# Optimization experiments

Hardware: AMD Instinct MI355X
Metric: run time of the kernel (lower is better)

The kernel has to match this reference:

```python
import jax, jax.numpy as jnp
from jax import lax
import numpy as np

B = 8; L = 1024; D_MODEL = 128; N_LAYER = 4
D_INNER = 256; D_STATE = 16; D_CONV = 4; DT_RANK = 8  # ceil(128/16)
N_STATE = 2; EPS = 1e-5


def setup_inputs() -> dict:
    key = jax.random.key(0)
    ks = jax.random.split(key, 9)
    s = 0.02
    return {
        "x": jax.random.normal(ks[0], (B, L, D_MODEL), jnp.float32),
        "in_proj_w": jax.random.normal(ks[1], (N_LAYER, 2 * D_INNER, D_MODEL), jnp.float32) * s,
        "conv_w": jax.random.normal(ks[2], (N_LAYER, D_INNER, 1, D_CONV), jnp.float32) * s,
        "conv_b": jnp.zeros((N_LAYER, D_INNER), jnp.float32),
        "x_proj_w": jax.random.normal(ks[3], (N_LAYER, DT_RANK + 2 * D_STATE, D_INNER), jnp.float32) * s,
        "dt_proj_w": jax.random.normal(ks[4], (N_LAYER, D_INNER, DT_RANK), jnp.float32) * s,
        "dt_proj_b": jax.random.normal(ks[5], (N_LAYER, D_INNER), jnp.float32) * s,
        "A_log": jnp.log(jnp.tile(jnp.arange(1, D_STATE + 1, dtype=jnp.float32), (N_LAYER, D_INNER, 1))),
        "D_param": jnp.ones((N_LAYER, D_INNER), jnp.float32),
        "out_proj_w": jax.random.normal(ks[6], (N_LAYER, D_MODEL, D_INNER), jnp.float32) * s,
        "norm_w": jnp.ones((N_LAYER, D_MODEL), jnp.float32),
        "norm_f_w": jnp.ones((D_MODEL,), jnp.float32),
        "bn_gamma": jnp.ones((D_MODEL,), jnp.float32),
        "bn_beta": jnp.zeros((D_MODEL,), jnp.float32),
        "head_w": jax.random.normal(ks[7], (N_STATE, D_MODEL), jnp.float32) * s,
        "head_b": jnp.zeros((N_STATE,), jnp.float32),
    }


def _rmsnorm(x, w):
    return x * lax.rsqrt(jnp.mean(x * x, axis=-1, keepdims=True) + EPS) * w


def _selective_scan(u, delta, A, Bm, Cm, D):
    # u, delta: (b,l,d); A: (d,n); Bm, Cm: (b,l,n); D: (d,)
    deltaA = jnp.exp(delta[..., None] * A)                          # (b,l,d,n)
    deltaBu = delta[..., None] * Bm[:, :, None, :] * u[..., None]   # (b,l,d,n)

    def step(h, t):
        dA, dBu, c = t
        h = dA * h + dBu                                            # (b,d,n)
        return h, jnp.einsum('bdn,bn->bd', h, c)

    h0 = jnp.zeros((u.shape[0], u.shape[2], A.shape[1]), u.dtype)
    _, ys = lax.scan(step, h0, (jnp.moveaxis(deltaA, 1, 0),
                                jnp.moveaxis(deltaBu, 1, 0),
                                jnp.moveaxis(Cm, 1, 0)))
    return jnp.moveaxis(ys, 0, 1) + u * D                           # (b,l,d)


def _mamba_block(x, in_w, cw, cb, xp_w, dt_w, dt_b, A_log, Dp, out_w):
    xz = jnp.einsum('bld,ed->ble', x, in_w)                         # (b,l,2*d_inner)
    xs, res = jnp.split(xz, 2, axis=-1)
    # depthwise causal conv, kernel D_CONV, left pad D_CONV-1 (matches pad=3 + truncate)
    xc = lax.conv_general_dilated(jnp.transpose(xs, (0, 2, 1)), cw, (1,),
                                  [(D_CONV - 1, 0)],
                                  dimension_numbers=('NCH', 'OIH', 'NCH'),
                                  feature_group_count=D_INNER)
    xs = jax.nn.silu(jnp.transpose(xc + cb[None, :, None], (0, 2, 1)))
    dbc = jnp.einsum('bld,ed->ble', xs, xp_w)
    dlt, Bm, Cm = jnp.split(dbc, [DT_RANK, DT_RANK + D_STATE], axis=-1)
    delta = jax.nn.softplus(jnp.einsum('blr,dr->bld', dlt, dt_w) + dt_b)
    A = -jnp.exp(A_log)
    y = _selective_scan(xs, delta, A, Bm, Cm, Dp)
    y = y * jax.nn.silu(res)
    return jnp.einsum('ble,de->bld', y, out_w)


def reference(x, in_proj_w, conv_w, conv_b, x_proj_w, dt_proj_w, dt_proj_b,
              A_log, D_param, out_proj_w, norm_w, norm_f_w,
              bn_gamma, bn_beta, head_w, head_b):
    h = x
    for i in range(N_LAYER):
        h = h + _mamba_block(_rmsnorm(h, norm_w[i]), in_proj_w[i], conv_w[i],
                             conv_b[i], x_proj_w[i], dt_proj_w[i], dt_proj_b[i],
                             A_log[i], D_param[i], out_proj_w[i])
    h = _rmsnorm(h, norm_f_w)
    feat = h[:, -1, :]                                              # (b, d_model)
    # BatchNorm1d (training mode: batch stats, biased variance), ReLU, Dropout(eval)=id
    mu = jnp.mean(feat, axis=0)
    var = jnp.mean((feat - mu) ** 2, axis=0)
    feat = (feat - mu) * lax.rsqrt(var + EPS) * bn_gamma + bn_beta
    feat = jax.nn.relu(feat)
    return feat @ head_w.T + head_b                                 # (b, n_state)
```

## Files before the change

kernel.cpp:

```cpp
#include <hip/hip_runtime.h>
#include <cstddef>

#define LQ 1024
#define DM 128
#define DI 256
#define DSN 16
#define NB 8
#define ROWS (NB*LQ)
#define EPSF 1e-5f
#define CHUNK 32
#define NCHUNK (LQ/CHUNK)

typedef _Float16 f16;
typedef __attribute__((ext_vector_type(8))) _Float16 f16x8;
typedef __attribute__((ext_vector_type(4))) _Float16 f16x4;
typedef __attribute__((ext_vector_type(4))) float f32x4;

static __device__ __forceinline__ float sigmoid_f(float x) { return 1.f/(1.f+__expf(-x)); }
static __device__ __forceinline__ float softplus_f(float x) {
  return (x > 20.f) ? x : log1pf(__expf(x));
}

__global__ __launch_bounds__(256) void cvt_all(
    const float* __restrict__ a, const float* __restrict__ bsrc, const float* __restrict__ csrc,
    f16* __restrict__ oa, f16* __restrict__ ob, f16* __restrict__ oc)
{
  int i = blockIdx.x*256 + threadIdx.x;
  const int na = (4*2*DI*DM)/4;
  const int nb = (4*40*DI)/4;
  const int nc = (4*DM*DI)/4;
  const float* s; f16* o; int k;
  if (i < na)            { s = a;    o = oa; k = i; }
  else if (i < na+nb)    { s = bsrc; o = ob; k = i - na; }
  else if (i < na+nb+nc) { s = csrc; o = oc; k = i - na - nb; }
  else return;
  float4 v = ((const float4*)s)[k];
  f16x4 r; r.x=(f16)v.x; r.y=(f16)v.y; r.z=(f16)v.z; r.w=(f16)v.w;
  ((f16x4*)o)[k] = r;
}

__global__ __launch_bounds__(256) void layer_front(
    const float* __restrict__ src, const float* __restrict__ nw,
    const f16* __restrict__ Win,
    const float* __restrict__ cw, const float* __restrict__ cb,
    const f16* __restrict__ xpw,
    const float* __restrict__ A_log,
    const float* __restrict__ dtw, const float* __restrict__ dtb,
    f16* __restrict__ xs_out, float* __restrict__ dbc_out,
    float* __restrict__ S, float* __restrict__ sumdl_out)
{
  __shared__ __align__(16) f16 Ah[48][136];
  __shared__ __align__(16) f16 sXc[48][264];
  __shared__ __align__(16) f16 sXs[32][264];
  __shared__ __align__(16) float sDbc[32][40];
  const int bc = blockIdx.x;
  const int b = bc >> 5, ck = bc & (NCHUNK-1);
  const int t0 = ck*CHUNK;
  const int tid = threadIdx.x;

  {
    const int r = tid >> 2;
    const int seg = (tid & 3) * 32;
    float4 v[8];
    float ss = 0.f;
    const bool valid = (r < 35) && (ck > 0 || r >= 3);
    if (valid) {
      const float* hr = src + (size_t)(b*LQ + t0 - 3 + r)*DM + seg;
      #pragma unroll
      for (int j = 0; j < 8; ++j) {
        v[j] = *(const float4*)(hr + j*4);
        ss += v[j].x*v[j].x + v[j].y*v[j].y + v[j].z*v[j].z + v[j].w*v[j].w;
      }
    }
    ss += __shfl_xor(ss, 1);
    ss += __shfl_xor(ss, 2);
    if (r < 48) {
      if (valid) {
        const float sc = rsqrtf(ss*(1.f/128.f) + EPSF);
        #pragma unroll
        for (int j = 0; j < 8; ++j) {
          float4 wv = *(const float4*)(nw + seg + j*4);
          f16x4 o;
          o.x=(f16)(v[j].x*sc*wv.x); o.y=(f16)(v[j].y*sc*wv.y);
          o.z=(f16)(v[j].z*sc*wv.z); o.w=(f16)(v[j].w*sc*wv.w);
          *(f16x4*)&Ah[r][seg + j*4] = o;
        }
      } else {
        #pragma unroll
        for (int j = 0; j < 8; ++j)
          *(f16x4*)&Ah[r][seg + j*4] = (f16x4){0,0,0,0};
      }
    }
  }
  __syncthreads();

  const int l = tid & 63, w = tid >> 6;
  const int fr = l & 15, kg = l >> 4;

  {
    f32x4 acc[3][4];
    #pragma unroll
    for (int m = 0; m < 3; ++m)
      #pragma unroll
      for (int n = 0; n < 4; ++n)
        acc[m][n] = (f32x4){0.f,0.f,0.f,0.f};
    #pragma unroll
    for (int s = 0; s < 4; ++s) {
      f16x8 af[3];
      #pragma unroll
      for (int m = 0; m < 3; ++m)
        af[m] = *(const f16x8*)&Ah[m*16 + fr][s*32 + kg*8];
      #pragma unroll
      for (int n = 0; n < 4; ++n) {
        f16x8 bfv = *(const f16x8*)(Win + (size_t)(w*64 + n*16 + fr)*DM + s*32 + kg*8);
        #pragma unroll
        for (int m = 0; m < 3; ++m)
          acc[m][n] = __builtin_amdgcn_mfma_f32_16x16x32_f16(af[m], bfv, acc[m][n], 0, 0, 0);
      }
    }
    #pragma unroll
    for (int m = 0; m < 3; ++m)
      #pragma unroll
      for (int n = 0; n < 4; ++n) {
        const int col = w*64 + n*16 + fr;
        #pragma unroll
        for (int j = 0; j < 4; ++j)
          sXc[m*16 + kg*4 + j][col] = (f16)acc[m][n][j];
      }
  }
  __syncthreads();

  {
    const int d = tid;
    const float4 cwv = *(const float4*)(cw + d*4);
    const float bias = cb[d];
    #pragma unroll 4
    for (int t = 0; t < CHUNK; ++t) {
      float a = bias + (float)sXc[t][d]*cwv.x + (float)sXc[t+1][d]*cwv.y
                     + (float)sXc[t+2][d]*cwv.z + (float)sXc[t+3][d]*cwv.w;
      float sv = a * sigmoid_f(a);
      f16 s16 = (f16)sv;
      sXs[t][d] = s16;
      xs_out[(size_t)(b*LQ + t0 + t)*DI + d] = s16;
    }
  }
  __syncthreads();

  if (w < 3) {
    f32x4 acc[2];
    acc[0] = (f32x4){0.f,0.f,0.f,0.f};
    acc[1] = (f32x4){0.f,0.f,0.f,0.f};
    const int wrow = w*16 + fr;
    #pragma unroll
    for (int s = 0; s < 8; ++s) {
      f16x8 bfv = (f16x8){0,0,0,0,0,0,0,0};
      if (wrow < 40) bfv = *(const f16x8*)(xpw + (size_t)wrow*DI + s*32 + kg*8);
      #pragma unroll
      for (int m = 0; m < 2; ++m) {
        f16x8 afv = *(const f16x8*)&sXs[m*16 + fr][s*32 + kg*8];
        acc[m] = __builtin_amdgcn_mfma_f32_16x16x32_f16(afv, bfv, acc[m], 0, 0, 0);
      }
    }
    if (wrow < 40) {
      #pragma unroll
      for (int m = 0; m < 2; ++m)
        #pragma unroll
        for (int j = 0; j < 4; ++j) {
          int row = m*16 + kg*4 + j;
          sDbc[row][wrow] = acc[m][j];
          dbc_out[(size_t)(b*LQ + t0 + row)*40 + wrow] = acc[m][j];
        }
    }
  }
  __syncthreads();

  {
    const int d = tid;
    float A[16];
    #pragma unroll
    for (int n = 0; n < 16; ++n) A[n] = -__expf(A_log[d*16+n]);
    const float4 dw0 = *(const float4*)(dtw + d*8);
    const float4 dw1 = *(const float4*)(dtw + d*8 + 4);
    const float bt = dtb[d];
    float h[16] = {};
    float sdl = 0.f;
    for (int t = 0; t < CHUNK; ++t) {
      float xa = bt + sDbc[t][0]*dw0.x + sDbc[t][1]*dw0.y + sDbc[t][2]*dw0.z + sDbc[t][3]*dw0.w
                    + sDbc[t][4]*dw1.x + sDbc[t][5]*dw1.y + sDbc[t][6]*dw1.z + sDbc[t][7]*dw1.w;
      float dl = softplus_f(xa);
      float uu = (float)sXs[t][d];
      float du = dl*uu;
      sdl += dl;
      #pragma unroll
      for (int n = 0; n < 16; ++n)
        h[n] = __expf(dl*A[n])*h[n] + du*sDbc[t][8+n];
    }
    float* Sp = S + ((size_t)bc*DI + d)*16;
    #pragma unroll
    for (int n = 0; n < 16; n += 4)
      *(float4*)(Sp+n) = make_float4(h[n],h[n+1],h[n+2],h[n+3]);
    sumdl_out[(size_t)bc*DI + d] = sdl;
  }
}

__global__ __launch_bounds__(256) void layer_back(
    const float* __restrict__ src, const float* __restrict__ nw,
    const f16* __restrict__ Win,
    const f16* __restrict__ xs, const float* __restrict__ dbc,
    const float* __restrict__ A_log,
    const float* __restrict__ dtw, const float* __restrict__ dtb,
    const float* __restrict__ Dp, const float* __restrict__ S,
    const float* __restrict__ sumdl, const f16* __restrict__ Wo,
    float* __restrict__ hout)
{
  __shared__ __align__(16) f16 Ah[32][136];
  __shared__ __align__(16) f16 sZ[32][264];
  __shared__ __align__(16) f16 sY[32][264];
  __shared__ float sB[CHUNK][16];
  __shared__ float sC[CHUNK][16];
  __shared__ float sDL[CHUNK][8];
  const int bc = blockIdx.x;
  const int b = bc >> 5, ck = bc & (NCHUNK-1);
  const int t0 = ck*CHUNK;
  const int tid = threadIdx.x;

  {
    const int r = tid >> 3;
    const int seg = (tid & 7) * 16;
    const float* hr = src + (size_t)(b*LQ + t0 + r)*DM + seg;
    float4 v[4];
    float ss = 0.f;
    #pragma unroll
    for (int j = 0; j < 4; ++j) {
      v[j] = *(const float4*)(hr + j*4);
      ss += v[j].x*v[j].x + v[j].y*v[j].y + v[j].z*v[j].z + v[j].w*v[j].w;
    }
    ss += __shfl_xor(ss, 1);
    ss += __shfl_xor(ss, 2);
    ss += __shfl_xor(ss, 4);
    const float sc = rsqrtf(ss*(1.f/128.f) + EPSF);
    #pragma unroll
    for (int j = 0; j < 4; ++j) {
      float4 wv = *(const float4*)(nw + seg + j*4);
      f16x4 o;
      o.x=(f16)(v[j].x*sc*wv.x); o.y=(f16)(v[j].y*sc*wv.y);
      o.z=(f16)(v[j].z*sc*wv.z); o.w=(f16)(v[j].w*sc*wv.w);
      *(f16x4*)&Ah[r][seg + j*4] = o;
    }
  }
  for (int e = tid; e < CHUNK*16; e += 256) {
    int t = e >> 4, n = e & 15;
    size_t r = (size_t)(b*LQ + t0 + t)*40;
    sB[t][n] = dbc[r + 8 + n];
    sC[t][n] = dbc[r + 24 + n];
  }
  for (int e = tid; e < CHUNK*8; e += 256) {
    int t = e >> 3, j = e & 7;
    sDL[t][j] = dbc[(size_t)(b*LQ + t0 + t)*40 + j];
  }
  __syncthreads();

  const int l = tid & 63, w = tid >> 6;
  const int fr = l & 15, kg = l >> 4;

  {
    f32x4 acc[2][4];
    #pragma unroll
    for (int m = 0; m < 2; ++m)
      #pragma unroll
      for (int n = 0; n < 4; ++n)
        acc[m][n] = (f32x4){0.f,0.f,0.f,0.f};
    #pragma unroll
    for (int s = 0; s < 4; ++s) {
      f16x8 af[2];
      #pragma unroll
      for (int m = 0; m < 2; ++m)
        af[m] = *(const f16x8*)&Ah[m*16 + fr][s*32 + kg*8];
      #pragma unroll
      for (int n = 0; n < 4; ++n) {
        f16x8 bfv = *(const f16x8*)(Win + (size_t)(DI + w*64 + n*16 + fr)*DM + s*32 + kg*8);
        #pragma unroll
        for (int m = 0; m < 2; ++m)
          acc[m][n] = __builtin_amdgcn_mfma_f32_16x16x32_f16(af[m], bfv, acc[m][n], 0, 0, 0);
      }
    }
    #pragma unroll
    for (int m = 0; m < 2; ++m)
      #pragma unroll
      for (int n = 0; n < 4; ++n) {
        const int col = w*64 + n*16 + fr;
        #pragma unroll
        for (int j = 0; j < 4; ++j)
          sZ[m*16 + kg*4 + j][col] = (f16)acc[m][n][j];
      }
  }

  const int d = tid;
  float A[16];
  #pragma unroll
  for (int n = 0; n < 16; ++n) A[n] = -__expf(A_log[d*16+n]);
  float h[16] = {};
  for (int c = 0; c < ck; ++c) {
    float sdl = sumdl[(size_t)(b*NCHUNK + c)*DI + d];
    const float* Sp = S + ((size_t)(b*NCHUNK + c)*DI + d)*16;
    #pragma unroll
    for (int n = 0; n < 16; n += 4) {
      float4 sv = *(const float4*)(Sp + n);
      h[n]   = __expf(A[n]  *sdl)*h[n]   + sv.x;
      h[n+1] = __expf(A[n+1]*sdl)*h[n+1] + sv.y;
      h[n+2] = __expf(A[n+2]*sdl)*h[n+2] + sv.z;
      h[n+3] = __expf(A[n+3]*sdl)*h[n+3] + sv.w;
    }
  }
  const float4 dw0 = *(const float4*)(dtw + d*8);
  const float4 dw1 = *(const float4*)(dtw + d*8 + 4);
  const float bt = dtb[d];
  const float Dv = Dp[d];
  __syncthreads();

  {
    const size_t ubase = (size_t)(b*LQ + t0)*DI + d;
    for (int t = 0; t < CHUNK; ++t) {
      float xa = bt + sDL[t][0]*dw0.x + sDL[t][1]*dw0.y + sDL[t][2]*dw0.z + sDL[t][3]*dw0.w
                    + sDL[t][4]*dw1.x + sDL[t][5]*dw1.y + sDL[t][6]*dw1.z + sDL[t][7]*dw1.w;
      float dl = softplus_f(xa);
      float uu = (float)xs[ubase + (size_t)t*DI];
      float du = dl*uu;
      float acc = uu*Dv;
      #pragma unroll
      for (int n = 0; n < 16; ++n) {
        h[n] = __expf(dl*A[n])*h[n] + du*sB[t][n];
        acc += h[n]*sC[t][n];
      }
      float res = (float)sZ[t][d];
      sY[t][d] = (f16)(acc * (res * sigmoid_f(res)));
    }
  }
  __syncthreads();

  {
    f16x8 bf[2][8];
    #pragma unroll
    for (int n = 0; n < 2; ++n)
      #pragma unroll
      for (int s = 0; s < 8; ++s)
        bf[n][s] = *(const f16x8*)(Wo + (size_t)(w*32 + n*16 + fr)*DI + s*32 + kg*8);
    f32x4 acc[2][2];
    #pragma unroll
    for (int m = 0; m < 2; ++m)
      #pragma unroll
      for (int n = 0; n < 2; ++n)
        acc[m][n] = (f32x4){0.f,0.f,0.f,0.f};
    #pragma unroll
    for (int s = 0; s < 8; ++s)
      #pragma unroll
      for (int m = 0; m < 2; ++m) {
        f16x8 afv = *(const f16x8*)&sY[m*16 + fr][s*32 + kg*8];
        #pragma unroll
        for (int n = 0; n < 2; ++n)
          acc[m][n] = __builtin_amdgcn_mfma_f32_16x16x32_f16(afv, bf[n][s], acc[m][n], 0, 0, 0);
      }
    #pragma unroll
    for (int m = 0; m < 2; ++m)
      #pragma unroll
      for (int n = 0; n < 2; ++n) {
        const int col = w*32 + n*16 + fr;
        #pragma unroll
        for (int j = 0; j < 4; ++j) {
          const int row = m*16 + kg*4 + j;
          const size_t gi = (size_t)(b*LQ + t0 + row)*DM + col;
          hout[gi] = acc[m][n][j] + src[gi];
        }
      }
  }
}

__global__ __launch_bounds__(256) void final_kernel(const float* __restrict__ h,
    const float* __restrict__ nfw, const float* __restrict__ gamma, const float* __restrict__ beta,
    const float* __restrict__ hw, const float* __restrict__ hb, float* __restrict__ out) {
  __shared__ float sf[8][128];
  __shared__ float sscale[8];
  int tid = threadIdx.x;
  for (int e = tid; e < 1024; e += 256) {
    int b = e >> 7, dd = e & 127;
    sf[b][dd] = h[((size_t)b*LQ + (LQ-1))*DM + dd];
  }
  __syncthreads();
  if (tid < 8) {
    float ss = 0.f;
    for (int dd = 0; dd < 128; ++dd) { float v = sf[tid][dd]; ss += v*v; }
    sscale[tid] = rsqrtf(ss/128.f + EPSF);
  }
  __syncthreads();
  for (int e = tid; e < 1024; e += 256) {
    int b = e >> 7, dd = e & 127;
    sf[b][dd] = sf[b][dd]*sscale[b]*nfw[dd];
  }
  __syncthreads();
  if (tid < 128) {
    float mu = 0.f;
    for (int b = 0; b < 8; ++b) mu += sf[b][tid];
    mu *= 0.125f;
    float var = 0.f;
    for (int b = 0; b < 8; ++b) { float dv = sf[b][tid]-mu; var += dv*dv; }
    var *= 0.125f;
    float rs = rsqrtf(var + EPSF);
    for (int b = 0; b < 8; ++b) {
      float v = (sf[b][tid]-mu)*rs*gamma[tid] + beta[tid];
      sf[b][tid] = v > 0.f ? v : 0.f;
    }
  }
  __syncthreads();
  if (tid < 16) {
    int b = tid >> 1, s = tid & 1;
    float acc = hb[s];
    for (int dd = 0; dd < 128; ++dd) acc += sf[b][dd]*hw[s*128+dd];
    out[b*2+s] = acc;
  }
}

extern "C" void kernel_launch(void* const* d_in, const int* in_sizes, int n_in,
                              void* d_out, int out_size, void* d_ws, size_t ws_size,
                              hipStream_t stream) {
  const float* x      = (const float*)d_in[0];
  const float* in_w   = (const float*)d_in[1];
  const float* conv_w = (const float*)d_in[2];
  const float* conv_b = (const float*)d_in[3];
  const float* xp_w   = (const float*)d_in[4];
  const float* dt_w   = (const float*)d_in[5];
  const float* dt_b   = (const float*)d_in[6];
  const float* A_log  = (const float*)d_in[7];
  const float* Dp     = (const float*)d_in[8];
  const float* out_w  = (const float*)d_in[9];
  const float* norm_w = (const float*)d_in[10];
  const float* norm_f = (const float*)d_in[11];
  const float* gamma  = (const float*)d_in[12];
  const float* beta   = (const float*)d_in[13];
  const float* head_w = (const float*)d_in[14];
  const float* head_b = (const float*)d_in[15];

  float* ws = (float*)d_ws;
  float* h     = ws;
  float* dbc   = h + (size_t)ROWS*DM;
  float* S     = dbc + (size_t)ROWS*40;
  float* sumdl = S + (size_t)NB*NCHUNK*DI*16;
  f16* xs     = (f16*)(sumdl + (size_t)NB*NCHUNK*DI);
  f16* wf_in  = xs + (size_t)ROWS*DI;
  f16* wf_xp  = wf_in + (size_t)4*2*DI*DM;
  f16* wf_out = wf_xp + (size_t)4*40*DI;

  cvt_all<<<424, 256, 0, stream>>>(in_w, xp_w, out_w, wf_in, wf_xp, wf_out);

  for (int layer = 0; layer < 4; ++layer) {
    const float* src = layer ? h : x;
    layer_front<<<NB*NCHUNK, 256, 0, stream>>>(
        src, norm_w + (size_t)layer*DM, wf_in + (size_t)layer*2*DI*DM,
        conv_w + (size_t)layer*DI*4, conv_b + (size_t)layer*DI,
        wf_xp + (size_t)layer*40*DI, A_log + (size_t)layer*DI*DSN,
        dt_w + (size_t)layer*DI*8, dt_b + (size_t)layer*DI,
        xs, dbc, S, sumdl);
    layer_back<<<NB*NCHUNK, 256, 0, stream>>>(
        src, norm_w + (size_t)layer*DM, wf_in + (size_t)layer*2*DI*DM,
        xs, dbc, A_log + (size_t)layer*DI*DSN,
        dt_w + (size_t)layer*DI*8, dt_b + (size_t)layer*DI,
        Dp + (size_t)layer*DI, S, sumdl,
        wf_out + (size_t)layer*DM*DI, h);
  }
  final_kernel<<<1, 256, 0, stream>>>(h, norm_f, gamma, beta, head_w, head_b, (float*)d_out);
}
```

Baseline: 313.3 us.

## Widen scan blocks to 1024 threads and add separate chunk-prefix kernel

Both layer kernels now launch 1024 threads per chunk block. Each d channel's 16-state scan is split across 4 threads with a shuffle reduction for the C contraction, and the MFMA tiles are redistributed over 16 waves. The O(ck) serial chunk-prefix loop in layer_back, previously recomputed by every block, is replaced by a dedicated scan_p2 kernel that computes each chunk's initial state once and writes it in place into S. The aim is more parallelism per block (only 256 blocks exist) and removal of redundant prefix work, at the cost of an extra launch per layer and more shuffles and syncs.

```diff
diff --git a/kernel.cpp b/kernel.cpp
--- a/kernel.cpp
+++ b/kernel.cpp
@@ -39,12 +39,10 @@
   ((f16x4*)o)[k] = r;
 }
 
-__global__ __launch_bounds__(256) void layer_front(
+__global__ __launch_bounds__(1024) void layer_front(
     const float* __restrict__ src, const float* __restrict__ nw,
-    const f16* __restrict__ Win,
-    const float* __restrict__ cw, const float* __restrict__ cb,
-    const f16* __restrict__ xpw,
-    const float* __restrict__ A_log,
+    const f16* __restrict__ Win, const float* __restrict__ cw, const float* __restrict__ cb,
+    const f16* __restrict__ xpw, const float* __restrict__ A_log,
     const float* __restrict__ dtw, const float* __restrict__ dtb,
     f16* __restrict__ xs_out, float* __restrict__ dbc_out,
     float* __restrict__ S, float* __restrict__ sumdl_out)
@@ -57,85 +55,66 @@
   const int b = bc >> 5, ck = bc & (NCHUNK-1);
   const int t0 = ck*CHUNK;
   const int tid = threadIdx.x;
-
-  {
-    const int r = tid >> 2;
-    const int seg = (tid & 3) * 32;
-    float4 v[8];
+  const int l = tid & 63, w = tid >> 6;
+  const int fr = l & 15, kg = l >> 4;
+
+  {
+    const int r = tid >> 4;
+    const int seg = (tid & 15) * 8;
+    float4 v0 = make_float4(0,0,0,0), v1 = v0;
+    const bool valid = (r < 35) && (ck > 0 || r >= 3);
     float ss = 0.f;
-    const bool valid = (r < 35) && (ck > 0 || r >= 3);
     if (valid) {
       const float* hr = src + (size_t)(b*LQ + t0 - 3 + r)*DM + seg;
-      #pragma unroll
-      for (int j = 0; j < 8; ++j) {
-        v[j] = *(const float4*)(hr + j*4);
-        ss += v[j].x*v[j].x + v[j].y*v[j].y + v[j].z*v[j].z + v[j].w*v[j].w;
-      }
-    }
-    ss += __shfl_xor(ss, 1);
-    ss += __shfl_xor(ss, 2);
+      v0 = *(const float4*)(hr);
+      v1 = *(const float4*)(hr + 4);
+      ss = v0.x*v0.x+v0.y*v0.y+v0.z*v0.z+v0.w*v0.w + v1.x*v1.x+v1.y*v1.y+v1.z*v1.z+v1.w*v1.w;
+    }
+    ss += __shfl_xor(ss, 1); ss += __shfl_xor(ss, 2);
+    ss += __shfl_xor(ss, 4); ss += __shfl_xor(ss, 8);
     if (r < 48) {
+      f16x4 o0 = (f16x4){0,0,0,0}, o1 = o0;
       if (valid) {
         const float sc = rsqrtf(ss*(1.f/128.f) + EPSF);
-        #pragma unroll
-        for (int j = 0; j < 8; ++j) {
-          float4 wv = *(const float4*)(nw + seg + j*4);
-          f16x4 o;
-          o.x=(f16)(v[j].x*sc*wv.x); o.y=(f16)(v[j].y*sc*wv.y);
-          o.z=(f16)(v[j].z*sc*wv.z); o.w=(f16)(v[j].w*sc*wv.w);
-          *(f16x4*)&Ah[r][seg + j*4] = o;
-        }
-      } else {
-        #pragma unroll
-        for (int j = 0; j < 8; ++j)
-          *(f16x4*)&Ah[r][seg + j*4] = (f16x4){0,0,0,0};
+        float4 w0 = *(const float4*)(nw + seg);
+        float4 w1 = *(const float4*)(nw + seg + 4);
+        o0.x=(f16)(v0.x*sc*w0.x); o0.y=(f16)(v0.y*sc*w0.y); o0.z=(f16)(v0.z*sc*w0.z); o0.w=(f16)(v0.w*sc*w0.w);
+        o1.x=(f16)(v1.x*sc*w1.x); o1.y=(f16)(v1.y*sc*w1.y); o1.z=(f16)(v1.z*sc*w1.z); o1.w=(f16)(v1.w*sc*w1.w);
       }
-    }
-  }
-  __syncthreads();
-
-  const int l = tid & 63, w = tid >> 6;
-  const int fr = l & 15, kg = l >> 4;
-
-  {
-    f32x4 acc[3][4];
+      *(f16x4*)&Ah[r][seg] = o0;
+      *(f16x4*)&Ah[r][seg+4] = o1;
+    }
+  }
+  __syncthreads();
+
+  {
+    f32x4 acc[3];
+    #pragma unroll
+    for (int m = 0; m < 3; ++m) acc[m] = (f32x4){0.f,0.f,0.f,0.f};
+    #pragma unroll
+    for (int s = 0; s < 4; ++s) {
+      f16x8 bfv = *(const f16x8*)(Win + (size_t)(w*16 + fr)*DM + s*32 + kg*8);
+      #pragma unroll
+      for (int m = 0; m < 3; ++m) {
+        f16x8 afv = *(const f16x8*)&Ah[m*16 + fr][s*32 + kg*8];
+        acc[m] = __builtin_amdgcn_mfma_f32_16x16x32_f16(afv, bfv, acc[m], 0, 0, 0);
+      }
+    }
     #pragma unroll
     for (int m = 0; m < 3; ++m)
       #pragma unroll
-      for (int n = 0; n < 4; ++n)
-        acc[m][n] = (f32x4){0.f,0.f,0.f,0.f};
-    #pragma unroll
-    for (int s = 0; s < 4; ++s) {
-      f16x8 af[3];
-      #pragma unroll
-      for (int m = 0; m < 3; ++m)
-        af[m] = *(const f16x8*)&Ah[m*16 + fr][s*32 + kg*8];
-      #pragma unroll
-      for (int n = 0; n < 4; ++n) {
-        f16x8 bfv = *(const f16x8*)(Win + (size_t)(w*64 + n*16 + fr)*DM + s*32 + kg*8);
-        #pragma unroll
-        for (int m = 0; m < 3; ++m)
-          acc[m][n] = __builtin_amdgcn_mfma_f32_16x16x32_f16(af[m], bfv, acc[m][n], 0, 0, 0);
-      }
-    }
-    #pragma unroll
-    for (int m = 0; m < 3; ++m)
-      #pragma unroll
-      for (int n = 0; n < 4; ++n) {
-        const int col = w*64 + n*16 + fr;
-        #pragma unroll
-        for (int j = 0; j < 4; ++j)
-          sXc[m*16 + kg*4 + j][col] = (f16)acc[m][n][j];
-      }
-  }
-  __syncthreads();
-
-  {
-    const int d = tid;
+      for (int j = 0; j < 4; ++j)
+        sXc[m*16 + kg*4 + j][w*16 + fr] = (f16)acc[m][j];
+  }
+  __syncthreads();
+
+  {
+    const int d = tid & 255, tq = tid >> 8;
     const float4 cwv = *(const float4*)(cw + d*4);
     const float bias = cb[d];
-    #pragma unroll 4
-    for (int t = 0; t < CHUNK; ++t) {
+    #pragma unroll
+    for (int i = 0; i < 8; ++i) {
+      int t = tq*8 + i;
       float a = bias + (float)sXc[t][d]*cwv.x + (float)sXc[t+1][d]*cwv.y
                      + (float)sXc[t+2][d]*cwv.z + (float)sXc[t+3][d]*cwv.w;
       float sv = a * sigmoid_f(a);
@@ -146,232 +125,194 @@
   }
   __syncthreads();
 
-  if (w < 3) {
-    f32x4 acc[2];
-    acc[0] = (f32x4){0.f,0.f,0.f,0.f};
-    acc[1] = (f32x4){0.f,0.f,0.f,0.f};
-    const int wrow = w*16 + fr;
+  if (w < 6) {
+    const int mi = w & 1, ni = w >> 1;
+    const int col = ni*16 + fr;
+    f32x4 acc = (f32x4){0.f,0.f,0.f,0.f};
     #pragma unroll
     for (int s = 0; s < 8; ++s) {
       f16x8 bfv = (f16x8){0,0,0,0,0,0,0,0};
-      if (wrow < 40) bfv = *(const f16x8*)(xpw + (size_t)wrow*DI + s*32 + kg*8);
-      #pragma unroll
-      for (int m = 0; m < 2; ++m) {
-        f16x8 afv = *(const f16x8*)&sXs[m*16 + fr][s*32 + kg*8];
-        acc[m] = __builtin_amdgcn_mfma_f32_16x16x32_f16(afv, bfv, acc[m], 0, 0, 0);
+      if (col < 40) bfv = *(const f16x8*)(xpw + (size_t)col*DI + s*32 + kg*8);
+      f16x8 afv = *(const f16x8*)&sXs[mi*16 + fr][s*32 + kg*8];
+      acc = __builtin_amdgcn_mfma_f32_16x16x32_f16(afv, bfv, acc, 0, 0, 0);
+    }
+    if (col < 40) {
+      #pragma unroll
+      for (int j = 0; j < 4; ++j) {
+        int row = mi*16 + kg*4 + j;
+        sDbc[row][col] = acc[j];
+        dbc_out[(size_t)(b*LQ + t0 + row)*40 + col] = acc[j];
       }
     }
-    if (wrow < 40) {
-      #pragma unroll
-      for (int m = 0; m < 2; ++m)
-        #pragma unroll
-        for (int j = 0; j < 4; ++j) {
-          int row = m*16 + kg*4 + j;
-          sDbc[row][wrow] = acc[m][j];
-          dbc_out[(size_t)(b*LQ + t0 + row)*40 + wrow] = acc[m][j];
-        }
-    }
-  }
-  __syncthreads();
-
-  {
-    const int d = tid;
-    float A[16];
-    #pragma unroll
-    for (int n = 0; n < 16; ++n) A[n] = -__expf(A_log[d*16+n]);
+  }
+  __syncthreads();
+
+  {
+    const int d = tid >> 2, g = tid & 3;
+    float A[4];
+    #pragma unroll
+    for (int j = 0; j < 4; ++j) A[j] = -__expf(A_log[d*16 + g*4 + j]);
     const float4 dw0 = *(const float4*)(dtw + d*8);
     const float4 dw1 = *(const float4*)(dtw + d*8 + 4);
     const float bt = dtb[d];
-    float h[16] = {};
+    float h[4] = {};
     float sdl = 0.f;
     for (int t = 0; t < CHUNK; ++t) {
       float xa = bt + sDbc[t][0]*dw0.x + sDbc[t][1]*dw0.y + sDbc[t][2]*dw0.z + sDbc[t][3]*dw0.w
                     + sDbc[t][4]*dw1.x + sDbc[t][5]*dw1.y + sDbc[t][6]*dw1.z + sDbc[t][7]*dw1.w;
       float dl = softplus_f(xa);
-      float uu = (float)sXs[t][d];
-      float du = dl*uu;
+      float du = dl * (float)sXs[t][d];
       sdl += dl;
       #pragma unroll
-      for (int n = 0; n < 16; ++n)
-        h[n] = __expf(dl*A[n])*h[n] + du*sDbc[t][8+n];
-    }
-    float* Sp = S + ((size_t)bc*DI + d)*16;
-    #pragma unroll
-    for (int n = 0; n < 16; n += 4)
-      *(float4*)(Sp+n) = make_float4(h[n],h[n+1],h[n+2],h[n+3]);
-    sumdl_out[(size_t)bc*DI + d] = sdl;
-  }
-}
-
-__global__ __launch_bounds__(256) void layer_back(
+      for (int j = 0; j < 4; ++j)
+        h[j] = __expf(dl*A[j])*h[j] + du*sDbc[t][8 + g*4 + j];
+    }
+    *(float4*)(S + ((size_t)bc*DI + d)*16 + g*4) = make_float4(h[0],h[1],h[2],h[3]);
+    if (g == 0) sumdl_out[(size_t)bc*DI + d] = sdl;
+  }
+}
+
+__global__ __launch_bounds__(256) void scan_p2(
+    float* __restrict__ S, const float* __restrict__ sumdl,
+    const float* __restrict__ A_log)
+{
+  int g = blockIdx.x*256 + threadIdx.x;
+  int b = g >> 12;
+  int dn = g & 4095;
+  float A = -__expf(A_log[dn]);
+  int d = dn >> 4;
+  float H = 0.f;
+  for (int c = 0; c < NCHUNK; ++c) {
+    size_t cidx = (size_t)(b*NCHUNK + c)*DI + d;
+    size_t idx = cidx*16 + (dn & 15);
+    float Sv = S[idx];
+    float P = __expf(A * sumdl[cidx]);
+    S[idx] = H;
+    H = P*H + Sv;
+  }
+}
+
+__global__ __launch_bounds__(1024) void layer_back(
     const float* __restrict__ src, const float* __restrict__ nw,
-    const f16* __restrict__ Win,
-    const f16* __restrict__ xs, const float* __restrict__ dbc,
-    const float* __restrict__ A_log,
+    const f16* __restrict__ Win, const f16* __restrict__ xs,
+    const float* __restrict__ dbc, const float* __restrict__ A_log,
     const float* __restrict__ dtw, const float* __restrict__ dtb,
-    const float* __restrict__ Dp, const float* __restrict__ S,
-    const float* __restrict__ sumdl, const f16* __restrict__ Wo,
-    float* __restrict__ hout)
+    const float* __restrict__ Dp, const float* __restrict__ Hinit,
+    const f16* __restrict__ Wo, float* __restrict__ hout)
 {
   __shared__ __align__(16) f16 Ah[32][136];
+  __shared__ __align__(16) f16 sXs[32][264];
   __shared__ __align__(16) f16 sZ[32][264];
   __shared__ __align__(16) f16 sY[32][264];
-  __shared__ float sB[CHUNK][16];
-  __shared__ float sC[CHUNK][16];
-  __shared__ float sDL[CHUNK][8];
+  __shared__ __align__(16) float sDbc[32][40];
   const int bc = blockIdx.x;
   const int b = bc >> 5, ck = bc & (NCHUNK-1);
   const int t0 = ck*CHUNK;
   const int tid = threadIdx.x;
-
-  {
-    const int r = tid >> 3;
-    const int seg = (tid & 7) * 16;
-    const float* hr = src + (size_t)(b*LQ + t0 + r)*DM + seg;
-    float4 v[4];
-    float ss = 0.f;
-    #pragma unroll
-    for (int j = 0; j < 4; ++j) {
-      v[j] = *(const float4*)(hr + j*4);
-      ss += v[j].x*v[j].x + v[j].y*v[j].y + v[j].z*v[j].z + v[j].w*v[j].w;
-    }
-    ss += __shfl_xor(ss, 1);
-    ss += __shfl_xor(ss, 2);
-    ss += __shfl_xor(ss, 4);
-    const float sc = rsqrtf(ss*(1.f/128.f) + EPSF);
-    #pragma unroll
-    for (int j = 0; j < 4; ++j) {
-      float4 wv = *(const float4*)(nw + seg + j*4);
-      f16x4 o;
-      o.x=(f16)(v[j].x*sc*wv.x); o.y=(f16)(v[j].y*sc*wv.y);
-      o.z=(f16)(v[j].z*sc*wv.z); o.w=(f16)(v[j].w*sc*wv.w);
-      *(f16x4*)&Ah[r][seg + j*4] = o;
-    }
-  }
-  for (int e = tid; e < CHUNK*16; e += 256) {
-    int t = e >> 4, n = e & 15;
-    size_t r = (size_t)(b*LQ + t0 + t)*40;
-    sB[t][n] = dbc[r + 8 + n];
-    sC[t][n] = dbc[r + 24 + n];
-  }
-  for (int e = tid; e < CHUNK*8; e += 256) {
-    int t = e >> 3, j = e & 7;
-    sDL[t][j] = dbc[(size_t)(b*LQ + t0 + t)*40 + j];
-  }
-  __syncthreads();
-
   const int l = tid & 63, w = tid >> 6;
   const int fr = l & 15, kg = l >> 4;
 
   {
-    f32x4 acc[2][4];
+    const int r = tid >> 5;
+    const int seg = (tid & 31) * 4;
+    const float* hr = src + (size_t)(b*LQ + t0 + r)*DM + seg;
+    float4 v = *(const float4*)hr;
+    float ss = v.x*v.x + v.y*v.y + v.z*v.z + v.w*v.w;
+    ss += __shfl_xor(ss, 1); ss += __shfl_xor(ss, 2);
+    ss += __shfl_xor(ss, 4); ss += __shfl_xor(ss, 8); ss += __shfl_xor(ss, 16);
+    const float sc = rsqrtf(ss*(1.f/128.f) + EPSF);
+    float4 wv = *(const float4*)(nw + seg);
+    f16x4 o;
+    o.x=(f16)(v.x*sc*wv.x); o.y=(f16)(v.y*sc*wv.y);
+    o.z=(f16)(v.z*sc*wv.z); o.w=(f16)(v.w*sc*wv.w);
+    *(f16x4*)&Ah[r][seg] = o;
+  }
+  {
+    const int r = tid >> 5, col = (tid & 31) * 8;
+    *(f16x8*)&sXs[r][col] = *(const f16x8*)(xs + (size_t)(b*LQ + t0 + r)*DI + col);
+  }
+  for (int e = tid; e < 32*40; e += 1024) {
+    int t = e / 40, c = e % 40;
+    sDbc[t][c] = dbc[(size_t)(b*LQ + t0 + t)*40 + c];
+  }
+  __syncthreads();
+
+  {
+    f32x4 acc[2];
+    acc[0] = (f32x4){0.f,0.f,0.f,0.f};
+    acc[1] = (f32x4){0.f,0.f,0.f,0.f};
+    #pragma unroll
+    for (int s = 0; s < 4; ++s) {
+      f16x8 bfv = *(const f16x8*)(Win + (size_t)(DI + w*16 + fr)*DM + s*32 + kg*8);
+      #pragma unroll
+      for (int m = 0; m < 2; ++m) {
+        f16x8 afv = *(const f16x8*)&Ah[m*16 + fr][s*32 + kg*8];
+        acc[m] = __builtin_amdgcn_mfma_f32_16x16x32_f16(afv, bfv, acc[m], 0, 0, 0);
+      }
+    }
     #pragma unroll
     for (int m = 0; m < 2; ++m)
       #pragma unroll
-      for (int n = 0; n < 4; ++n)
-        acc[m][n] = (f32x4){0.f,0.f,0.f,0.f};
-    #pragma unroll
-    for (int s = 0; s < 4; ++s) {
-      f16x8 af[2];
-      #pragma unroll
-      for (int m = 0; m < 2; ++m)
-        af[m] = *(const f16x8*)&Ah[m*16 + fr][s*32 + kg*8];
-      #pragma unroll
-      for (int n = 0; n < 4; ++n) {
-        f16x8 bfv = *(const f16x8*)(Win + (size_t)(DI + w*64 + n*16 + fr)*DM + s*32 + kg*8);
-        #pragma unroll
-        for (int m = 0; m < 2; ++m)
-          acc[m][n] = __builtin_amdgcn_mfma_f32_16x16x32_f16(af[m], bfv, acc[m][n], 0, 0, 0);
-      }
-    }
-    #pragma unroll
-    for (int m = 0; m < 2; ++m)
-      #pragma unroll
-      for (int n = 0; n < 4; ++n) {
-        const int col = w*64 + n*16 + fr;
-        #pragma unroll
-        for (int j = 0; j < 4; ++j)
-          sZ[m*16 + kg*4 + j][col] = (f16)acc[m][n][j];
-      }
-  }
-
-  const int d = tid;
-  float A[16];
+      for (int j = 0; j < 4; ++j)
+        sZ[m*16 + kg*4 + j][w*16 + fr] = (f16)acc[m][j];
+  }
+
+  const int d = tid >> 2, g = tid & 3;
+  float A[4];
   #pragma unroll
-  for (int n = 0; n < 16; ++n) A[n] = -__expf(A_log[d*16+n]);
-  float h[16] = {};
-  for (int c = 0; c < ck; ++c) {
-    float sdl = sumdl[(size_t)(b*NCHUNK + c)*DI + d];
-    const float* Sp = S + ((size_t)(b*NCHUNK + c)*DI + d)*16;
-    #pragma unroll
-    for (int n = 0; n < 16; n += 4) {
-      float4 sv = *(const float4*)(Sp + n);
-      h[n]   = __expf(A[n]  *sdl)*h[n]   + sv.x;
-      h[n+1] = __expf(A[n+1]*sdl)*h[n+1] + sv.y;
-      h[n+2] = __expf(A[n+2]*sdl)*h[n+2] + sv.z;
-      h[n+3] = __expf(A[n+3]*sdl)*h[n+3] + sv.w;
-    }
+  for (int j = 0; j < 4; ++j) A[j] = -__expf(A_log[d*16 + g*4 + j]);
+  float h[4];
+  {
+    float4 hv = *(const float4*)(Hinit + ((size_t)bc*DI + d)*16 + g*4);
+    h[0]=hv.x; h[1]=hv.y; h[2]=hv.z; h[3]=hv.w;
   }
   const float4 dw0 = *(const float4*)(dtw + d*8);
   const float4 dw1 = *(const float4*)(dtw + d*8 + 4);
   const float bt = dtb[d];
   const float Dv = Dp[d];
-  __syncthreads();
-
-  {
-    const size_t ubase = (size_t)(b*LQ + t0)*DI + d;
-    for (int t = 0; t < CHUNK; ++t) {
-      float xa = bt + sDL[t][0]*dw0.x + sDL[t][1]*dw0.y + sDL[t][2]*dw0.z + sDL[t][3]*dw0.w
-                    + sDL[t][4]*dw1.x + sDL[t][5]*dw1.y + sDL[t][6]*dw1.z + sDL[t][7]*dw1.w;
-      float dl = softplus_f(xa);
-      float uu = (float)xs[ubase + (size_t)t*DI];
-      float du = dl*uu;
-      float acc = uu*Dv;
-      #pragma unroll
-      for (int n = 0; n < 16; ++n) {
-        h[n] = __expf(dl*A[n])*h[n] + du*sB[t][n];
-        acc += h[n]*sC[t][n];
-      }
+
+  const int mi = w & 1, ni = w >> 1;
+  f16x8 bf[8];
+  #pragma unroll
+  for (int s = 0; s < 8; ++s)
+    bf[s] = *(const f16x8*)(Wo + (size_t)(ni*16 + fr)*DI + s*32 + kg*8);
+  __syncthreads();
+
+  for (int t = 0; t < CHUNK; ++t) {
+    float xa = bt + sDbc[t][0]*dw0.x + sDbc[t][1]*dw0.y + sDbc[t][2]*dw0.z + sDbc[t][3]*dw0.w
+                  + sDbc[t][4]*dw1.x + sDbc[t][5]*dw1.y + sDbc[t][6]*dw1.z + sDbc[t][7]*dw1.w;
+    float dl = softplus_f(xa);
+    float uu = (float)sXs[t][d];
+    float du = dl*uu;
+    float pacc = 0.f;
+    #pragma unroll
+    for (int j = 0; j < 4; ++j) {
+      h[j] = __expf(dl*A[j])*h[j] + du*sDbc[t][8 + g*4 + j];
+      pacc += h[j]*sDbc[t][24 + g*4 + j];
+    }
+    pacc += __shfl_xor(pacc, 1);
+    pacc += __shfl_xor(pacc, 2);
+    if (g == 0) {
       float res = (float)sZ[t][d];
-      sY[t][d] = (f16)(acc * (res * sigmoid_f(res)));
-    }
-  }
-  __syncthreads();
-
-  {
-    f16x8 bf[2][8];
-    #pragma unroll
-    for (int n = 0; n < 2; ++n)
-      #pragma unroll
-      for (int s = 0; s < 8; ++s)
-        bf[n][s] = *(const f16x8*)(Wo + (size_t)(w*32 + n*16 + fr)*DI + s*32 + kg*8);
-    f32x4 acc[2][2];
-    #pragma unroll
-    for (int m = 0; m < 2; ++m)
-      #pragma unroll
-      for (int n = 0; n < 2; ++n)
-        acc[m][n] = (f32x4){0.f,0.f,0.f,0.f};
-    #pragma unroll
-    for (int s = 0; s < 8; ++s)
-      #pragma unroll
-      for (int m = 0; m < 2; ++m) {
-        f16x8 afv = *(const f16x8*)&sY[m*16 + fr][s*32 + kg*8];
-        #pragma unroll
-        for (int n = 0; n < 2; ++n)
-          acc[m][n] = __builtin_amdgcn_mfma_f32_16x16x32_f16(afv, bf[n][s], acc[m][n], 0, 0, 0);
-      }
-    #pragma unroll
-    for (int m = 0; m < 2; ++m)
-      #pragma unroll
-      for (int n = 0; n < 2; ++n) {
-        const int col = w*32 + n*16 + fr;
-        #pragma unroll
-        for (int j = 0; j < 4; ++j) {
-          const int row = m*16 + kg*4 + j;
-          const size_t gi = (size_t)(b*LQ + t0 + row)*DM + col;
-          hout[gi] = acc[m][n][j] + src[gi];
-        }
-      }
+      sY[t][d] = (f16)((pacc + uu*Dv) * (res * sigmoid_f(res)));
+    }
+  }
+  __syncthreads();
+
+  {
+    f32x4 acc = (f32x4){0.f,0.f,0.f,0.f};
+    #pragma unroll
+    for (int s = 0; s < 8; ++s) {
+      f16x8 afv = *(const f16x8*)&sY[mi*16 + fr][s*32 + kg*8];
+      acc = __builtin_amdgcn_mfma_f32_16x16x32_f16(afv, bf[s], acc, 0, 0, 0);
+    }
+    const int col = ni*16 + fr;
+    #pragma unroll
+    for (int j = 0; j < 4; ++j) {
+      const int row = mi*16 + kg*4 + j;
+      const size_t gi = (size_t)(b*LQ + t0 + row)*DM + col;
+      hout[gi] = acc[j] + src[gi];
+    }
   }
 }
 
@@ -453,17 +394,18 @@
 
   for (int layer = 0; layer < 4; ++layer) {
     const float* src = layer ? h : x;
-    layer_front<<<NB*NCHUNK, 256, 0, stream>>>(
+    layer_front<<<NB*NCHUNK, 1024, 0, stream>>>(
         src, norm_w + (size_t)layer*DM, wf_in + (size_t)layer*2*DI*DM,
         conv_w + (size_t)layer*DI*4, conv_b + (size_t)layer*DI,
         wf_xp + (size_t)layer*40*DI, A_log + (size_t)layer*DI*DSN,
         dt_w + (size_t)layer*DI*8, dt_b + (size_t)layer*DI,
         xs, dbc, S, sumdl);
-    layer_back<<<NB*NCHUNK, 256, 0, stream>>>(
+    scan_p2<<<NB*DI*DSN/256, 256, 0, stream>>>(S, sumdl, A_log + (size_t)layer*DI*DSN);
+    layer_back<<<NB*NCHUNK, 1024, 0, stream>>>(
         src, norm_w + (size_t)layer*DM, wf_in + (size_t)layer*2*DI*DM,
         xs, dbc, A_log + (size_t)layer*DI*DSN,
         dt_w + (size_t)layer*DI*8, dt_b + (size_t)layer*DI,
-        Dp + (size_t)layer*DI, S, sumdl,
+        Dp + (size_t)layer*DI, S,
         wf_out + (size_t)layer*DM*DI, h);
   }
   final_kernel<<<1, 256, 0, stream>>>(h, norm_f, gamma, beta, head_w, head_b, (float*)d_out);
```

Result: slower. 401.9 us (+28.3%).
